# Kernel optimization log

Measured on AMD Instinct MI355X. Metric: run time of the kernel, lower is better.

Reference implementation:

```python
import jax, jax.numpy as jnp
import numpy as np

NUM_SLOTS = 3
NUM_ORIENTS = 8
PATCH_SIZE = 81  # 9x9 board
BUY_SIZE = NUM_SLOTS * NUM_ORIENTS * PATCH_SIZE  # 1944
ACTIONS = 1 + PATCH_SIZE + BUY_SIZE  # 2026
NEG = -1.0e9
EPS = 1e-5

B = 4096
C_IN = 256
HID = 256


def setup_inputs() -> dict:
    key = jax.random.key(0)
    ks = jax.random.split(key, 12)
    s = 0.05
    return {
        "x": jax.random.normal(ks[0], (B, C_IN, 9, 9), jnp.float32),
        "action_mask": jax.random.randint(ks[1], (B, ACTIONS), 0, 2, dtype=jnp.int32),
        # p_conv: 1x1 conv, no bias (use_batch_norm=True) -> weight (HID, C_IN)
        "conv_w": jax.random.normal(ks[2], (HID, C_IN), jnp.float32) * s,
        # BatchNorm2d (inference form with running stats)
        "bn_gamma": jnp.ones((HID,), jnp.float32),
        "bn_beta": jnp.zeros((HID,), jnp.float32),
        "bn_mean": jax.random.normal(ks[3], (HID,), jnp.float32) * 0.1,
        "bn_var": jax.random.uniform(ks[4], (HID,), jnp.float32, 0.5, 1.5),
        "type_w": jax.random.normal(ks[5], (3, HID), jnp.float32) * s,
        "type_b": jnp.zeros((3,), jnp.float32),
        "patch_w": jax.random.normal(ks[6], (1, HID), jnp.float32) * s,
        "patch_b": jnp.zeros((1,), jnp.float32),
        "slot_w": jax.random.normal(ks[7], (NUM_SLOTS, HID), jnp.float32) * s,
        "slot_b": jnp.zeros((NUM_SLOTS,), jnp.float32),
        "orient_w": jax.random.normal(ks[8], (NUM_SLOTS * NUM_ORIENTS, HID), jnp.float32) * s,
        "orient_b": jnp.zeros((NUM_SLOTS * NUM_ORIENTS,), jnp.float32),
        "pos_w": jax.random.normal(ks[9], (NUM_SLOTS * NUM_ORIENTS, HID), jnp.float32) * s,
        "pos_b": jnp.zeros((NUM_SLOTS * NUM_ORIENTS,), jnp.float32),
    }


def _masked_logsoftmax(logits, mask_bool):
    lg = jnp.where(mask_bool, logits, NEG)
    return jnp.maximum(jax.nn.log_softmax(lg, axis=-1), -100.0)


def reference(x, action_mask, conv_w, bn_gamma, bn_beta, bn_mean, bn_var,
              type_w, type_b, patch_w, patch_b, slot_w, slot_b,
              orient_w, orient_b, pos_w, pos_b):
    b = x.shape[0]
    # 1x1 conv + BN (eval) + ReLU
    p = jnp.einsum('bchw,oc->bohw', x, conv_w)
    scale = bn_gamma * jax.lax.rsqrt(bn_var + EPS)
    p = jax.nn.relu(p * scale[None, :, None, None] + (bn_beta - bn_mean * scale)[None, :, None, None])
    p_mean = p.mean(axis=(2, 3))  # (B, HID)

    # masks from action_mask layout [pass | 81 patch | 1944 buy]
    am = action_mask > 0
    patch_mask = am[:, 1:1 + PATCH_SIZE]
    buy4d = am[:, 82:82 + BUY_SIZE].reshape(b, NUM_SLOTS, NUM_ORIENTS, PATCH_SIZE)
    type_mask = jnp.stack([am[:, 0], patch_mask.any(-1), buy4d.reshape(b, -1).any(-1)], axis=-1)
    orient_mask = buy4d.any(-1)
    slot_mask = orient_mask.any(-1)

    type_lp = _masked_logsoftmax(p_mean @ type_w.T + type_b, type_mask)          # (B,3)
    patch_logits = jnp.einsum('bchw,oc->bohw', p, patch_w).reshape(b, PATCH_SIZE) \
        + patch_b[0]
    patch_lp = _masked_logsoftmax(patch_logits, patch_mask)                       # (B,81)
    slot_lp = _masked_logsoftmax(p_mean @ slot_w.T + slot_b, slot_mask)           # (B,3)
    orient_lp = _masked_logsoftmax(
        (p_mean @ orient_w.T + orient_b).reshape(b, NUM_SLOTS, NUM_ORIENTS), orient_mask)
    pos_logits = (jnp.einsum('bchw,oc->bohw', p, pos_w) + pos_b[None, :, None, None]) \
        .reshape(b, NUM_SLOTS, NUM_ORIENTS, PATCH_SIZE)
    pos_lp = _masked_logsoftmax(pos_logits, buy4d)                                # (B,3,8,81)

    pass_lp = type_lp[:, 0:1]
    patch_joint = type_lp[:, 1:2] + patch_lp
    buy_joint = (type_lp[:, 2:3, None, None] + slot_lp[:, :, None, None]
                 + orient_lp[:, :, :, None] + pos_lp).reshape(b, BUY_SIZE)
    return jnp.concatenate([pass_lp, patch_joint, buy_joint], axis=1)  # (B, 2026)
```

## Files before the change

### kernel.cpp

```cpp
#include <hip/hip_runtime.h>

#define ACT 2026
#define NEGV -1.0e9f

typedef short short8 __attribute__((ext_vector_type(8)));
typedef float f32x4 __attribute__((ext_vector_type(4)));

__device__ __forceinline__ unsigned f2bf(float f) {
  unsigned u = __float_as_uint(f);
  return (u + 0x7FFFu + ((u >> 16) & 1u)) >> 16;
}

__device__ __forceinline__ unsigned cvtpk(float lo, float hi) {
  unsigned r;
  asm("v_cvt_pk_bf16_f32 %0, %1, %2" : "=v"(r) : "v"(lo), "v"(hi));
  return r;
}

#define GL16(gp, lp) __builtin_amdgcn_global_load_lds(                         \
    (const __attribute__((address_space(1))) void*)(gp),                       \
    (__attribute__((address_space(3))) void*)(lp), 16, 0, 0)

__global__ void prep_w_kernel(const float* __restrict__ conv_w,
                              const float* __restrict__ pos_w,
                              const float* __restrict__ patch_w,
                              unsigned short* __restrict__ wimg,
                              unsigned short* __restrict__ w2img) {
  int g = blockIdx.x * 256 + threadIdx.x;
  if (g < 8192) {
    int r = g & 15, gq = (g >> 4) & 3, mtg = (g >> 6) & 15, ks = g >> 10;
    const float* src = conv_w + (mtg * 16 + r) * 256 + ks * 32 + gq * 8;
    unsigned v0 = f2bf(src[0]) | (f2bf(src[1]) << 16);
    unsigned v1 = f2bf(src[2]) | (f2bf(src[3]) << 16);
    unsigned v2 = f2bf(src[4]) | (f2bf(src[5]) << 16);
    unsigned v3 = f2bf(src[6]) | (f2bf(src[7]) << 16);
    uint4 q; q.x = v0; q.y = v1; q.z = v2; q.w = v3;
    *(uint4*)(wimg + g * 8) = q;
  } else if (g < 9216) {
    int g2 = g - 8192;
    int r = g2 & 15, gq = (g2 >> 4) & 3, mt = (g2 >> 6) & 1, ks2 = g2 >> 7;
    int m2 = mt * 16 + r;
    int o0 = ks2 * 32 + gq * 8;
    unsigned short v[8];
#pragma unroll
    for (int e = 0; e < 8; ++e) {
      float f = 0.f;
      if (m2 < 24) f = pos_w[m2 * 256 + o0 + e];
      else if (m2 == 24) f = patch_w[o0 + e];
      v[e] = (unsigned short)f2bf(f);
    }
    uint4 q;
    q.x = (unsigned)v[0] | ((unsigned)v[1] << 16);
    q.y = (unsigned)v[2] | ((unsigned)v[3] << 16);
    q.z = (unsigned)v[4] | ((unsigned)v[5] << 16);
    q.w = (unsigned)v[6] | ((unsigned)v[7] << 16);
    *(uint4*)(w2img + g2 * 8) = q;
  }
}

__global__ __launch_bounds__(512, 4)
void policy_main(const float* __restrict__ x,
                 const int* __restrict__ am,
                 const unsigned short* __restrict__ wimg,
                 const unsigned short* __restrict__ w2img,
                 const float* __restrict__ bn_gamma, const float* __restrict__ bn_beta,
                 const float* __restrict__ bn_mean, const float* __restrict__ bn_var,
                 const float* __restrict__ type_w, const float* __restrict__ type_b,
                 const float* __restrict__ patch_b,
                 const float* __restrict__ slot_w, const float* __restrict__ slot_b,
                 const float* __restrict__ orient_w, const float* __restrict__ orient_b,
                 const float* __restrict__ pos_b,
                 float* __restrict__ out)
{
  __shared__ __align__(16) char s_big[49152];
  __shared__ __align__(16) float s_scale[256];
  __shared__ __align__(16) float s_bias[256];
  __shared__ __align__(16) float s_pmean[256];
  __shared__ float s_part[240];
  __shared__ float s_hl[30];
  __shared__ float s_tlp[3], s_slp[3], s_olp[24];
  __shared__ int s_omask[24];
  __shared__ int s_misc[6];

  char* f32buf = s_big;
  char* bfimg  = s_big + 31104;
  unsigned short* pT = (unsigned short*)s_big;
  float* s_out2 = (float*)s_big;

  const int tid = threadIdx.x;
  const int w  = tid >> 6;
  const int l  = tid & 63;
  const int b  = blockIdx.x;
  const float* xb = x + (size_t)b * (256 * 81);

  if (tid < 256) {
    float sc = bn_gamma[tid] * rsqrtf(bn_var[tid] + 1e-5f);
    s_scale[tid] = sc;
    s_bias[tid]  = bn_beta[tid] - bn_mean[tid] * sc;
  }

  const int kg = l >> 4;
  const int kr = l & 15;
  const int g4 = kg * 4;

  f32x4 acc[2][6];
#pragma unroll
  for (int i = 0; i < 2; ++i)
#pragma unroll
    for (int j = 0; j < 6; ++j) {
      f32x4 z = {0.f, 0.f, 0.f, 0.f};
      acc[i][j] = z;
    }

  auto STAGE = [&](int ks) {
    const char* g = (const char*)xb + ks * 10368;
    char* lb = f32buf + (ks % 3) * 10368;
    int o1 = w * 81;
    int o2 = o1 + 17;
    GL16(g + (o1 + l) * 16, lb + o1 * 16);
    GL16(g + (o2 + l) * 16, lb + o2 * 16);
  };

  auto TRANSPOSE = [&](int t) {
    const float* src = (const float*)(f32buf + (t % 3) * 10368);
    char* dst = bfimg + (t & 1) * 6144;
    if (tid < 384) {
      int q = tid;
      int nt_ = q >> 6, kr_ = (q >> 2) & 15, kg_ = q & 3;
      const float* s = src + kg_ * 648 + nt_ * 16 + kr_;
      uint4 v;
      v.x = cvtpk(s[0],   s[81]);
      v.y = cvtpk(s[162], s[243]);
      v.z = cvtpk(s[324], s[405]);
      v.w = cvtpk(s[486], s[567]);
      *(uint4*)(dst + q * 16) = v;
    }
  };

  STAGE(0); STAGE(1); STAGE(2);
  asm volatile("s_waitcnt vmcnt(4)" ::: "memory");
  __builtin_amdgcn_s_barrier();
  __builtin_amdgcn_sched_barrier(0);
  TRANSPOSE(0);
  asm volatile("s_waitcnt vmcnt(2)" ::: "memory");
  asm volatile("s_waitcnt lgkmcnt(0)" ::: "memory");
  __builtin_amdgcn_s_barrier();
  __builtin_amdgcn_sched_barrier(0);

  const int fragoff = (kr * 4 + kg) * 16;

  auto STEP = [&](int k) {
    short8 af[2];
    {
      const unsigned short* ab = wimg + k * 8192 + w * 1024 + kg * 128 + kr * 8;
      af[0] = *(const short8*)(ab);
      af[1] = *(const short8*)(ab + 512);
    }
    __builtin_amdgcn_sched_barrier(0);
    if (k + 3 < 8) STAGE(k + 3);
    if (k + 1 < 8) TRANSPOSE(k + 1);
    const char* bi = bfimg + (k & 1) * 6144;
#pragma unroll
    for (int nt = 0; nt < 6; ++nt) {
      short8 bf = *(const short8*)(bi + nt * 1024 + fragoff);
      acc[0][nt] = __builtin_amdgcn_mfma_f32_16x16x32_bf16(af[0], bf, acc[0][nt], 0, 0, 0);
      acc[1][nt] = __builtin_amdgcn_mfma_f32_16x16x32_bf16(af[1], bf, acc[1][nt], 0, 0, 0);
    }
    if (k < 7) {
      if (k + 3 < 8) asm volatile("s_waitcnt vmcnt(2)" ::: "memory");
      else           asm volatile("s_waitcnt vmcnt(0)" ::: "memory");
      asm volatile("s_waitcnt lgkmcnt(0)" ::: "memory");
      __builtin_amdgcn_s_barrier();
      __builtin_amdgcn_sched_barrier(0);
    } else {
      __syncthreads();
    }
  };

  STEP(0); STEP(1); STEP(2); STEP(3);
  STEP(4); STEP(5); STEP(6); STEP(7);

#pragma unroll
  for (int mi = 0; mi < 2; ++mi) {
    int ob = w * 32 + mi * 16 + g4;
    float sc0 = s_scale[ob], sc1 = s_scale[ob + 1], sc2 = s_scale[ob + 2], sc3 = s_scale[ob + 3];
    float bi0 = s_bias[ob],  bi1 = s_bias[ob + 1],  bi2 = s_bias[ob + 2],  bi3 = s_bias[ob + 3];
    float vs0 = 0.f, vs1 = 0.f, vs2 = 0.f, vs3 = 0.f;
    int ks2 = ob >> 5;
    int j2  = (ob >> 3) & 3;
    int e0  = ob & 7;
    char* pbase = (char*)pT + ks2 * 6144 + j2 * 256 + kr * 16 + e0 * 2;
#pragma unroll
    for (int nt = 0; nt < 6; ++nt) {
      float v0 = fmaxf(acc[mi][nt][0] * sc0 + bi0, 0.f);
      float v1 = fmaxf(acc[mi][nt][1] * sc1 + bi1, 0.f);
      float v2 = fmaxf(acc[mi][nt][2] * sc2 + bi2, 0.f);
      float v3 = fmaxf(acc[mi][nt][3] * sc3 + bi3, 0.f);
      if (nt < 5 || kr == 0) { vs0 += v0; vs1 += v1; vs2 += v2; vs3 += v3; }
      uint2 pvv;
      pvv.x = cvtpk(v0, v1);
      pvv.y = cvtpk(v2, v3);
      *(uint2*)(pbase + nt * 1024) = pvv;
    }
    float vv[4] = {vs0, vs1, vs2, vs3};
#pragma unroll
    for (int i = 0; i < 4; ++i) {
      float s = vv[i];
      s += __shfl_xor(s, 1);
      s += __shfl_xor(s, 2);
      s += __shfl_xor(s, 4);
      s += __shfl_xor(s, 8);
      vv[i] = s;
    }
    if (kr == 0) {
      s_pmean[ob]     = vv[0] * (1.f / 81.f);
      s_pmean[ob + 1] = vv[1] * (1.f / 81.f);
      s_pmean[ob + 2] = vv[2] * (1.f / 81.f);
      s_pmean[ob + 3] = vv[3] * (1.f / 81.f);
    }
  }
  __syncthreads();

  const int* amr = am + (size_t)b * ACT;
  const int mt  = w & 1;
  const int ntb = (w >> 1) * 3;
  f32x4 acc2[3];
#pragma unroll
  for (int t = 0; t < 3; ++t) { f32x4 z = {0.f, 0.f, 0.f, 0.f}; acc2[t] = z; }

  if (w < 4) {
#pragma unroll
    for (int ks2 = 0; ks2 < 8; ++ks2) {
      const unsigned short* ap = w2img + ((ks2 * 2 + mt) * 4 + kg) * 128 + kr * 8;
      short8 a2 = *(const short8*)ap;
#pragma unroll
      for (int t = 0; t < 3; ++t) {
        const short8* bp = (const short8*)((const char*)pT + ks2 * 6144 + (ntb + t) * 1024 + kg * 256 + kr * 16);
        acc2[t] = __builtin_amdgcn_mfma_f32_16x16x32_bf16(a2, *bp, acc2[t], 0, 0, 0);
      }
    }
  } else {
    for (int t = w - 4; t < 25; t += 4) {
      int off = (t < 24) ? (82 + t * 81) : 1;
      int v1 = amr[off + l];
      int v2 = (l < 17) ? amr[off + 64 + l] : 0;
      unsigned long long bal = __ballot((v1 | v2) != 0);
      if (l == 0) {
        int any = (bal != 0ULL) ? 1 : 0;
        if (t < 24) s_omask[t] = any; else s_misc[0] = any;
      }
    }
    int hh = tid - 256;
    if (hh < 240) {
      int h = hh >> 3, seg = hh & 7;
      const float* wp = (h < 3) ? (type_w + h * 256)
                      : (h < 6) ? (slot_w + (h - 3) * 256)
                                : (orient_w + (h - 6) * 256);
      float p = 0.f;
      int base = seg * 32;
#pragma unroll 8
      for (int e = 0; e < 32; ++e) p += s_pmean[base + e] * wp[base + e];
      s_part[hh] = p;
    }
  }
  __syncthreads();

  if (w < 4) {
#pragma unroll
    for (int t = 0; t < 3; ++t) {
      int hw = (ntb + t) * 16 + kr;
      int m2 = mt * 16 + g4;
#pragma unroll
      for (int i = 0; i < 4; ++i)
        s_out2[(m2 + i) * 104 + hw] = acc2[t][i];
    }
  }
  if (tid < 30) {
    float a = 0.f;
#pragma unroll
    for (int e = 0; e < 8; ++e) a += s_part[tid * 8 + e];
    a += (tid < 3) ? type_b[tid] : (tid < 6) ? slot_b[tid - 3] : orient_b[tid - 6];
    s_hl[tid] = a;
  }
  if (tid == 32) {
    int sa0 = 0, sa1 = 0, sa2 = 0;
#pragma unroll
    for (int r = 0; r < 8; ++r) { sa0 |= s_omask[r]; sa1 |= s_omask[8 + r]; sa2 |= s_omask[16 + r]; }
    s_misc[1] = sa0; s_misc[2] = sa1; s_misc[3] = sa2;
    s_misc[4] = sa0 | sa1 | sa2;
  }
  __syncthreads();

  if (tid == 0) {
    int mk0 = amr[0] > 0, mk1 = s_misc[0], mk2 = s_misc[4];
    float g0 = mk0 ? s_hl[0] : NEGV;
    float g1 = mk1 ? s_hl[1] : NEGV;
    float g2 = mk2 ? s_hl[2] : NEGV;
    float m = fmaxf(fmaxf(g0, g1), g2);
    float sum = __expf(g0 - m) + __expf(g1 - m) + __expf(g2 - m);
    float ls = m + __logf(sum);
    s_tlp[0] = fmaxf(g0 - ls, -100.f);
    s_tlp[1] = fmaxf(g1 - ls, -100.f);
    s_tlp[2] = fmaxf(g2 - ls, -100.f);
  } else if (tid == 1) {
    float g[3]; float m = -3.0e38f;
#pragma unroll
    for (int s = 0; s < 3; ++s) { g[s] = s_misc[1 + s] ? s_hl[3 + s] : NEGV; m = fmaxf(m, g[s]); }
    float sum = 0.f;
#pragma unroll
    for (int s = 0; s < 3; ++s) sum += __expf(g[s] - m);
    float ls = m + __logf(sum);
#pragma unroll
    for (int s = 0; s < 3; ++s) s_slp[s] = fmaxf(g[s] - ls, -100.f);
  } else if (tid >= 2 && tid < 5) {
    int s = tid - 2;
    float g[8]; float m = -3.0e38f;
#pragma unroll
    for (int r = 0; r < 8; ++r) { g[r] = s_omask[s * 8 + r] ? s_hl[6 + s * 8 + r] : NEGV; m = fmaxf(m, g[r]); }
    float sum = 0.f;
#pragma unroll
    for (int r = 0; r < 8; ++r) sum += __expf(g[r] - m);
    float ls = m + __logf(sum);
#pragma unroll
    for (int r = 0; r < 8; ++r) s_olp[s * 8 + r] = fmaxf(g[r] - ls, -100.f);
  }
  __syncthreads();

  float* ob_out = out + (size_t)b * ACT;
  for (int t = w; t < 25; t += 8) {
    int off = (t < 24) ? (82 + t * 81) : 1;
    float badd = (t < 24) ? pos_b[t] : patch_b[0];
    int a1 = amr[off + l];
    int a2v = (l < 17) ? amr[off + 64 + l] : 0;
    float lg1 = (a1 > 0) ? (s_out2[t * 104 + l] + badd) : NEGV;
    float lg2 = (l < 17 && a2v > 0) ? (s_out2[t * 104 + 64 + l] + badd) : NEGV;
    float mx = fmaxf(lg1, (l < 17) ? lg2 : -3.0e38f);
#pragma unroll
    for (int mm = 1; mm < 64; mm <<= 1) mx = fmaxf(mx, __shfl_xor(mx, mm));
    float sm = __expf(lg1 - mx) + ((l < 17) ? __expf(lg2 - mx) : 0.f);
#pragma unroll
    for (int mm = 1; mm < 64; mm <<= 1) sm += __shfl_xor(sm, mm);
    float lse = mx + __logf(sm);
    float lp1 = fmaxf(lg1 - lse, -100.f);
    float lp2 = fmaxf(lg2 - lse, -100.f);
    float addj; int obase;
    if (t < 24) { addj = s_tlp[2] + s_slp[t >> 3] + s_olp[t]; obase = 82 + t * 81; }
    else        { addj = s_tlp[1];                             obase = 1; }
    ob_out[obase + l] = addj + lp1;
    if (l < 17) ob_out[obase + 64 + l] = addj + lp2;
    if (t == 24 && l == 0) ob_out[0] = s_tlp[0];
  }
}

extern "C" void kernel_launch(void* const* d_in, const int* in_sizes, int n_in,
                              void* d_out, int out_size, void* d_ws, size_t ws_size,
                              hipStream_t stream) {
  (void)in_sizes; (void)n_in; (void)out_size; (void)ws_size;
  const float* x        = (const float*)d_in[0];
  const int*   amask    = (const int*)d_in[1];
  const float* conv_w   = (const float*)d_in[2];
  const float* bn_gamma = (const float*)d_in[3];
  const float* bn_beta  = (const float*)d_in[4];
  const float* bn_mean  = (const float*)d_in[5];
  const float* bn_var   = (const float*)d_in[6];
  const float* type_w   = (const float*)d_in[7];
  const float* type_b   = (const float*)d_in[8];
  const float* patch_w  = (const float*)d_in[9];
  const float* patch_b  = (const float*)d_in[10];
  const float* slot_w   = (const float*)d_in[11];
  const float* slot_b   = (const float*)d_in[12];
  const float* orient_w = (const float*)d_in[13];
  const float* orient_b = (const float*)d_in[14];
  const float* pos_w    = (const float*)d_in[15];
  const float* pos_b    = (const float*)d_in[16];
  float* outp = (float*)d_out;

  unsigned short* wimg  = (unsigned short*)d_ws;
  unsigned short* w2img = wimg + 65536;

  prep_w_kernel<<<36, 256, 0, stream>>>(conv_w, pos_w, patch_w, wimg, w2img);
  policy_main<<<4096, 512, 0, stream>>>(x, amask, wimg, w2img,
                                        bn_gamma, bn_beta, bn_mean, bn_var,
                                        type_w, type_b, patch_b,
                                        slot_w, slot_b, orient_w, orient_b,
                                        pos_b, outp);
}
```

Baseline: 194.9 us.

## Load whole input tile directly to registers, convert to bf16 once, drop staged pipeline

Replaces the three-buffer global_load_lds staging plus per-step transpose pipeline with a single upfront phase. In that phase each thread loads its input elements straight from global memory into registers, converts them to bf16 and writes the full 48KB bf16 image to LDS. The main MFMA loop then runs all 8 k-steps with no barriers, double-buffering only the weight fragments in registers. This removes per-step barriers and waitcnts, but loses the overlap between global loads and MFMA work and uses strided scalar global loads that may coalesce poorly.

```diff
diff --git a/kernel.cpp b/kernel.cpp
--- a/kernel.cpp
+++ b/kernel.cpp
@@ -16,10 +16,6 @@
   asm("v_cvt_pk_bf16_f32 %0, %1, %2" : "=v"(r) : "v"(lo), "v"(hi));
   return r;
 }
-
-#define GL16(gp, lp) __builtin_amdgcn_global_load_lds(                         \
-    (const __attribute__((address_space(1))) void*)(gp),                       \
-    (__attribute__((address_space(3))) void*)(lp), 16, 0, 0)
 
 __global__ void prep_w_kernel(const float* __restrict__ conv_w,
                               const float* __restrict__ pos_w,
@@ -82,8 +78,7 @@
   __shared__ int s_omask[24];
   __shared__ int s_misc[6];
 
-  char* f32buf = s_big;
-  char* bfimg  = s_big + 31104;
+  char* bfimg = s_big;
   unsigned short* pT = (unsigned short*)s_big;
   float* s_out2 = (float*)s_big;
 
@@ -93,6 +88,37 @@
   const int b  = blockIdx.x;
   const float* xb = x + (size_t)b * (256 * 81);
 
+  {
+    const int pkg = l & 3;
+    const int pkr = (l >> 2) & 15;
+    const float* sp[6];
+    int dof[6];
+#pragma unroll
+    for (int j = 0; j < 6; ++j) {
+      int ksnt = j * 8 + w;
+      int ks = ksnt / 6, nt = ksnt % 6;
+      int hwj = nt * 16 + pkr;
+      if (hwj > 80) hwj = 80;
+      sp[j]  = xb + (ks * 32 + pkg * 8) * 81 + hwj;
+      dof[j] = ks * 6144 + nt * 1024 + (pkr * 4 + pkg) * 16;
+    }
+    float fb[6][8];
+#pragma unroll
+    for (int j = 0; j < 6; ++j)
+#pragma unroll
+      for (int e = 0; e < 8; ++e)
+        fb[j][e] = sp[j][e * 81];
+#pragma unroll
+    for (int j = 0; j < 6; ++j) {
+      uint4 v;
+      v.x = cvtpk(fb[j][0], fb[j][1]);
+      v.y = cvtpk(fb[j][2], fb[j][3]);
+      v.z = cvtpk(fb[j][4], fb[j][5]);
+      v.w = cvtpk(fb[j][6], fb[j][7]);
+      *(uint4*)(bfimg + dof[j]) = v;
+    }
+  }
+
   if (tid < 256) {
     float sc = bn_gamma[tid] * rsqrtf(bn_var[tid] + 1e-5f);
     s_scale[tid] = sc;
@@ -102,6 +128,7 @@
   const int kg = l >> 4;
   const int kr = l & 15;
   const int g4 = kg * 4;
+  const int fragoff = (kr * 4 + kg) * 16;
 
   f32x4 acc[2][6];
 #pragma unroll
@@ -112,73 +139,34 @@
       acc[i][j] = z;
     }
 
-  auto STAGE = [&](int ks) {
-    const char* g = (const char*)xb + ks * 10368;
-    char* lb = f32buf + (ks % 3) * 10368;
-    int o1 = w * 81;
-    int o2 = o1 + 17;
-    GL16(g + (o1 + l) * 16, lb + o1 * 16);
-    GL16(g + (o2 + l) * 16, lb + o2 * 16);
+  __syncthreads();
+
+  auto LDA = [&](int ks, short8 (&d)[2]) {
+    const unsigned short* ab = wimg + ks * 8192 + w * 1024 + kg * 128 + kr * 8;
+    d[0] = *(const short8*)(ab);
+    d[1] = *(const short8*)(ab + 512);
   };
 
-  auto TRANSPOSE = [&](int t) {
-    const float* src = (const float*)(f32buf + (t % 3) * 10368);
-    char* dst = bfimg + (t & 1) * 6144;
-    if (tid < 384) {
-      int q = tid;
-      int nt_ = q >> 6, kr_ = (q >> 2) & 15, kg_ = q & 3;
-      const float* s = src + kg_ * 648 + nt_ * 16 + kr_;
-      uint4 v;
-      v.x = cvtpk(s[0],   s[81]);
-      v.y = cvtpk(s[162], s[243]);
-      v.z = cvtpk(s[324], s[405]);
-      v.w = cvtpk(s[486], s[567]);
-      *(uint4*)(dst + q * 16) = v;
-    }
-  };
-
-  STAGE(0); STAGE(1); STAGE(2);
-  asm volatile("s_waitcnt vmcnt(4)" ::: "memory");
-  __builtin_amdgcn_s_barrier();
-  __builtin_amdgcn_sched_barrier(0);
-  TRANSPOSE(0);
-  asm volatile("s_waitcnt vmcnt(2)" ::: "memory");
-  asm volatile("s_waitcnt lgkmcnt(0)" ::: "memory");
-  __builtin_amdgcn_s_barrier();
-  __builtin_amdgcn_sched_barrier(0);
-
-  const int fragoff = (kr * 4 + kg) * 16;
-
-  auto STEP = [&](int k) {
-    short8 af[2];
-    {
-      const unsigned short* ab = wimg + k * 8192 + w * 1024 + kg * 128 + kr * 8;
-      af[0] = *(const short8*)(ab);
-      af[1] = *(const short8*)(ab + 512);
-    }
-    __builtin_amdgcn_sched_barrier(0);
-    if (k + 3 < 8) STAGE(k + 3);
-    if (k + 1 < 8) TRANSPOSE(k + 1);
-    const char* bi = bfimg + (k & 1) * 6144;
+  short8 afA[2], afB[2];
+  LDA(0, afA);
+
+  auto STEP = [&](int k, short8 (&cur)[2], short8 (&nxt)[2]) {
+    if (k < 7) LDA(k + 1, nxt);
+    const char* bi = bfimg + k * 6144;
 #pragma unroll
     for (int nt = 0; nt < 6; ++nt) {
       short8 bf = *(const short8*)(bi + nt * 1024 + fragoff);
-      acc[0][nt] = __builtin_amdgcn_mfma_f32_16x16x32_bf16(af[0], bf, acc[0][nt], 0, 0, 0);
-      acc[1][nt] = __builtin_amdgcn_mfma_f32_16x16x32_bf16(af[1], bf, acc[1][nt], 0, 0, 0);
-    }
-    if (k < 7) {
-      if (k + 3 < 8) asm volatile("s_waitcnt vmcnt(2)" ::: "memory");
-      else           asm volatile("s_waitcnt vmcnt(0)" ::: "memory");
-      asm volatile("s_waitcnt lgkmcnt(0)" ::: "memory");
-      __builtin_amdgcn_s_barrier();
-      __builtin_amdgcn_sched_barrier(0);
-    } else {
-      __syncthreads();
+      acc[0][nt] = __builtin_amdgcn_mfma_f32_16x16x32_bf16(cur[0], bf, acc[0][nt], 0, 0, 0);
+      acc[1][nt] = __builtin_amdgcn_mfma_f32_16x16x32_bf16(cur[1], bf, acc[1][nt], 0, 0, 0);
     }
   };
 
-  STEP(0); STEP(1); STEP(2); STEP(3);
-  STEP(4); STEP(5); STEP(6); STEP(7);
+  STEP(0, afA, afB); STEP(1, afB, afA);
+  STEP(2, afA, afB); STEP(3, afB, afA);
+  STEP(4, afA, afB); STEP(5, afB, afA);
+  STEP(6, afA, afB); STEP(7, afB, afA);
+
+  __syncthreads();
 
 #pragma unroll
   for (int mi = 0; mi < 2; ++mi) {
```

After: 233.5 us. 19.8% more time.

## Deepen input pipeline to four stages and process two K-steps per barrier

Applied to the files above, without the earlier changes.

Expands the staging ring to four fp32 x buffers and four bf16 transposed images, so two K-slices are transposed and consumed per barrier, halving barrier count. Raises wave priority around the MFMA loops. Computes the type/slot/orient log-softmaxes redundantly in registers instead of via shared memory, removing one block barrier. The larger LDS footprint may reduce resident blocks per CU.

```diff
diff --git a/kernel.cpp b/kernel.cpp
--- a/kernel.cpp
+++ b/kernel.cpp
@@ -72,18 +72,17 @@
                  const float* __restrict__ pos_b,
                  float* __restrict__ out)
 {
-  __shared__ __align__(16) char s_big[49152];
+  __shared__ __align__(16) char s_big[66048];
   __shared__ __align__(16) float s_scale[256];
   __shared__ __align__(16) float s_bias[256];
   __shared__ __align__(16) float s_pmean[256];
   __shared__ float s_part[240];
   __shared__ float s_hl[30];
-  __shared__ float s_tlp[3], s_slp[3], s_olp[24];
   __shared__ int s_omask[24];
   __shared__ int s_misc[6];
 
   char* f32buf = s_big;
-  char* bfimg  = s_big + 31104;
+  char* bfimg  = s_big + 41472;
   unsigned short* pT = (unsigned short*)s_big;
   float* s_out2 = (float*)s_big;
 
@@ -102,6 +101,7 @@
   const int kg = l >> 4;
   const int kr = l & 15;
   const int g4 = kg * 4;
+  const int fragoff = (kr * 4 + kg) * 16;
 
   f32x4 acc[2][6];
 #pragma unroll
@@ -114,61 +114,76 @@
 
   auto STAGE = [&](int ks) {
     const char* g = (const char*)xb + ks * 10368;
-    char* lb = f32buf + (ks % 3) * 10368;
+    char* lb = f32buf + (ks & 3) * 10368;
     int o1 = w * 81;
     int o2 = o1 + 17;
     GL16(g + (o1 + l) * 16, lb + o1 * 16);
     GL16(g + (o2 + l) * 16, lb + o2 * 16);
   };
 
-  auto TRANSPOSE = [&](int t) {
-    const float* src = (const float*)(f32buf + (t % 3) * 10368);
-    char* dst = bfimg + (t & 1) * 6144;
-    if (tid < 384) {
-      int q = tid;
-      int nt_ = q >> 6, kr_ = (q >> 2) & 15, kg_ = q & 3;
-      const float* s = src + kg_ * 648 + nt_ * 16 + kr_;
-      uint4 v;
-      v.x = cvtpk(s[0],   s[81]);
-      v.y = cvtpk(s[162], s[243]);
-      v.z = cvtpk(s[324], s[405]);
-      v.w = cvtpk(s[486], s[567]);
-      *(uint4*)(dst + q * 16) = v;
-    }
+  auto TRX = [&](int t, int q) {
+    const float* src = (const float*)(f32buf + (t & 3) * 10368);
+    char* dst = bfimg + (t & 3) * 6144;
+    int nt_ = q >> 6, kr_ = (q >> 2) & 15, kg_ = q & 3;
+    const float* s = src + kg_ * 648 + nt_ * 16 + kr_;
+    uint4 v;
+    v.x = cvtpk(s[0],   s[81]);
+    v.y = cvtpk(s[162], s[243]);
+    v.z = cvtpk(s[324], s[405]);
+    v.w = cvtpk(s[486], s[567]);
+    *(uint4*)(dst + q * 16) = v;
   };
-
-  STAGE(0); STAGE(1); STAGE(2);
+  auto TRANSPOSE2 = [&](int tA, int tB) {
+    if (tid < 384) TRX(tA, tid);
+    else           TRX(tB, tid - 384);
+    if (tid < 256) TRX(tB, 128 + tid);
+  };
+
+  STAGE(0); STAGE(1); STAGE(2); STAGE(3);
   asm volatile("s_waitcnt vmcnt(4)" ::: "memory");
   __builtin_amdgcn_s_barrier();
   __builtin_amdgcn_sched_barrier(0);
-  TRANSPOSE(0);
-  asm volatile("s_waitcnt vmcnt(2)" ::: "memory");
+  TRANSPOSE2(0, 1);
+  asm volatile("s_waitcnt vmcnt(0)" ::: "memory");
   asm volatile("s_waitcnt lgkmcnt(0)" ::: "memory");
   __builtin_amdgcn_s_barrier();
   __builtin_amdgcn_sched_barrier(0);
 
-  const int fragoff = (kr * 4 + kg) * 16;
-
-  auto STEP = [&](int k) {
-    short8 af[2];
+  auto SUPER = [&](int s) {
+    const int t0 = 2 * s, t1 = t0 + 1;
+    short8 af[4];
     {
-      const unsigned short* ab = wimg + k * 8192 + w * 1024 + kg * 128 + kr * 8;
-      af[0] = *(const short8*)(ab);
-      af[1] = *(const short8*)(ab + 512);
+      const unsigned short* ab0 = wimg + t0 * 8192 + w * 1024 + kg * 128 + kr * 8;
+      const unsigned short* ab1 = wimg + t1 * 8192 + w * 1024 + kg * 128 + kr * 8;
+      af[0] = *(const short8*)(ab0);
+      af[1] = *(const short8*)(ab0 + 512);
+      af[2] = *(const short8*)(ab1);
+      af[3] = *(const short8*)(ab1 + 512);
     }
     __builtin_amdgcn_sched_barrier(0);
-    if (k + 3 < 8) STAGE(k + 3);
-    if (k + 1 < 8) TRANSPOSE(k + 1);
-    const char* bi = bfimg + (k & 1) * 6144;
+    if (s < 2) {
+      STAGE(t0 + 4);
+      STAGE(t1 + 4);
+    }
+    if (s < 3) TRANSPOSE2(t0 + 2, t1 + 2);
+    const char* bi0 = bfimg + (t0 & 3) * 6144;
+    const char* bi1 = bfimg + (t1 & 3) * 6144;
+    __builtin_amdgcn_s_setprio(1);
 #pragma unroll
     for (int nt = 0; nt < 6; ++nt) {
-      short8 bf = *(const short8*)(bi + nt * 1024 + fragoff);
+      short8 bf = *(const short8*)(bi0 + nt * 1024 + fragoff);
       acc[0][nt] = __builtin_amdgcn_mfma_f32_16x16x32_bf16(af[0], bf, acc[0][nt], 0, 0, 0);
       acc[1][nt] = __builtin_amdgcn_mfma_f32_16x16x32_bf16(af[1], bf, acc[1][nt], 0, 0, 0);
     }
-    if (k < 7) {
-      if (k + 3 < 8) asm volatile("s_waitcnt vmcnt(2)" ::: "memory");
-      else           asm volatile("s_waitcnt vmcnt(0)" ::: "memory");
+#pragma unroll
+    for (int nt = 0; nt < 6; ++nt) {
+      short8 bf = *(const short8*)(bi1 + nt * 1024 + fragoff);
+      acc[0][nt] = __builtin_amdgcn_mfma_f32_16x16x32_bf16(af[2], bf, acc[0][nt], 0, 0, 0);
+      acc[1][nt] = __builtin_amdgcn_mfma_f32_16x16x32_bf16(af[3], bf, acc[1][nt], 0, 0, 0);
+    }
+    __builtin_amdgcn_s_setprio(0);
+    if (s < 3) {
+      asm volatile("s_waitcnt vmcnt(0)" ::: "memory");
       asm volatile("s_waitcnt lgkmcnt(0)" ::: "memory");
       __builtin_amdgcn_s_barrier();
       __builtin_amdgcn_sched_barrier(0);
@@ -177,8 +192,7 @@
     }
   };
 
-  STEP(0); STEP(1); STEP(2); STEP(3);
-  STEP(4); STEP(5); STEP(6); STEP(7);
+  SUPER(0); SUPER(1); SUPER(2); SUPER(3);
 
 #pragma unroll
   for (int mi = 0; mi < 2; ++mi) {
@@ -285,24 +299,26 @@
   if (tid == 32) {
     int sa0 = 0, sa1 = 0, sa2 = 0;
 #pragma unroll
-    for (int r = 0; r < 8; ++r) { sa0 |= s_omask[r]; sa1 |= s_omask[8 + r]; sa2 |= s_omask[16 + r]; }
+    for (int rr = 0; rr < 8; ++rr) { sa0 |= s_omask[rr]; sa1 |= s_omask[8 + rr]; sa2 |= s_omask[16 + rr]; }
     s_misc[1] = sa0; s_misc[2] = sa1; s_misc[3] = sa2;
     s_misc[4] = sa0 | sa1 | sa2;
   }
   __syncthreads();
 
-  if (tid == 0) {
+  float tlp0, tlp1, tlp2;
+  {
     int mk0 = amr[0] > 0, mk1 = s_misc[0], mk2 = s_misc[4];
     float g0 = mk0 ? s_hl[0] : NEGV;
     float g1 = mk1 ? s_hl[1] : NEGV;
     float g2 = mk2 ? s_hl[2] : NEGV;
     float m = fmaxf(fmaxf(g0, g1), g2);
-    float sum = __expf(g0 - m) + __expf(g1 - m) + __expf(g2 - m);
-    float ls = m + __logf(sum);
-    s_tlp[0] = fmaxf(g0 - ls, -100.f);
-    s_tlp[1] = fmaxf(g1 - ls, -100.f);
-    s_tlp[2] = fmaxf(g2 - ls, -100.f);
-  } else if (tid == 1) {
+    float ls = m + __logf(__expf(g0 - m) + __expf(g1 - m) + __expf(g2 - m));
+    tlp0 = fmaxf(g0 - ls, -100.f);
+    tlp1 = fmaxf(g1 - ls, -100.f);
+    tlp2 = fmaxf(g2 - ls, -100.f);
+  }
+  float slp[3];
+  {
     float g[3]; float m = -3.0e38f;
 #pragma unroll
     for (int s = 0; s < 3; ++s) { g[s] = s_misc[1 + s] ? s_hl[3 + s] : NEGV; m = fmaxf(m, g[s]); }
@@ -311,20 +327,8 @@
     for (int s = 0; s < 3; ++s) sum += __expf(g[s] - m);
     float ls = m + __logf(sum);
 #pragma unroll
-    for (int s = 0; s < 3; ++s) s_slp[s] = fmaxf(g[s] - ls, -100.f);
-  } else if (tid >= 2 && tid < 5) {
-    int s = tid - 2;
-    float g[8]; float m = -3.0e38f;
-#pragma unroll
-    for (int r = 0; r < 8; ++r) { g[r] = s_omask[s * 8 + r] ? s_hl[6 + s * 8 + r] : NEGV; m = fmaxf(m, g[r]); }
-    float sum = 0.f;
-#pragma unroll
-    for (int r = 0; r < 8; ++r) sum += __expf(g[r] - m);
-    float ls = m + __logf(sum);
-#pragma unroll
-    for (int r = 0; r < 8; ++r) s_olp[s * 8 + r] = fmaxf(g[r] - ls, -100.f);
-  }
-  __syncthreads();
+    for (int s = 0; s < 3; ++s) slp[s] = fmaxf(g[s] - ls, -100.f);
+  }
 
   float* ob_out = out + (size_t)b * ACT;
   for (int t = w; t < 25; t += 8) {
@@ -344,11 +348,28 @@
     float lp1 = fmaxf(lg1 - lse, -100.f);
     float lp2 = fmaxf(lg2 - lse, -100.f);
     float addj; int obase;
-    if (t < 24) { addj = s_tlp[2] + s_slp[t >> 3] + s_olp[t]; obase = 82 + t * 81; }
-    else        { addj = s_tlp[1];                             obase = 1; }
+    if (t < 24) {
+      int sl = t >> 3;
+      float g[8]; float m = -3.0e38f;
+#pragma unroll
+      for (int rr = 0; rr < 8; ++rr) {
+        g[rr] = s_omask[sl * 8 + rr] ? s_hl[6 + sl * 8 + rr] : NEGV;
+        m = fmaxf(m, g[rr]);
+      }
+      float sum = 0.f;
+#pragma unroll
+      for (int rr = 0; rr < 8; ++rr) sum += __expf(g[rr] - m);
+      float ls = m + __logf(sum);
+      float olp_t = fmaxf(g[t & 7] - ls, -100.f);
+      addj = tlp2 + slp[sl] + olp_t;
+      obase = 82 + t * 81;
+    } else {
+      addj = tlp1;
+      obase = 1;
+    }
     ob_out[obase + l] = addj + lp1;
     if (l < 17) ob_out[obase + 64 + l] = addj + lp2;
-    if (t == 24 && l == 0) ob_out[0] = s_tlp[0];
+    if (t == 24 && l == 0) ob_out[0] = tlp0;
   }
 }
 
```

After: 193.9 us. About the same (-0.5%).
